# Kernel tuning notes

Measured on AMD Instinct MI355X. Metric: run time of the kernel, lower is better.

Reference implementation:

```python
import jax, jax.numpy as jnp
import numpy as np

N, E, B = 50000, 500000, 32
FEAT, HID, EDGE_DIM = 64, 128, 16
NUM_TASKS, TED, NCLS, TASKS_PER = 5000, 64, 3, 8
NLAYERS = 2


def setup_inputs() -> dict:
    key = jax.random.key(0)
    ks = jax.random.split(key, 20)
    s = 0.05
    inp = {
        "h": jax.random.normal(ks[0], (N, FEAT), jnp.float32),
        "x": jax.random.normal(ks[1], (N, 3), jnp.float32),
        "edge_index": jax.random.randint(ks[2], (2, E), 0, N, dtype=jnp.int32),
        "edge_attr": jax.random.normal(ks[3], (E, EDGE_DIM), jnp.float32),
        "batch": (jnp.arange(N, dtype=jnp.int32) * B // N).astype(jnp.int32),
        "tasks_indices": jnp.stack([
            jnp.repeat(jnp.arange(B, dtype=jnp.int32), TASKS_PER),
            jax.random.randint(ks[4], (B * TASKS_PER,), 0, NUM_TASKS, dtype=jnp.int32),
        ], axis=1),
        "batch_size": B,
        "embed_W": jax.random.normal(ks[5], (FEAT, HID), jnp.float32) * s,
        "embed_b": jnp.zeros((HID,), jnp.float32),
        "res_W": jax.random.normal(ks[6], (NLAYERS, HID, HID), jnp.float32) * s,
        "msg_W": jax.random.normal(ks[7], (NLAYERS, 2 * HID + 1, HID), jnp.float32) * s,
        "msg_b": jnp.zeros((NLAYERS, HID), jnp.float32),
        "upd_W": jax.random.normal(ks[8], (NLAYERS, 2 * HID, HID), jnp.float32) * s,
        "upd_b": jnp.zeros((NLAYERS, HID), jnp.float32),
        "mlp_W0": jax.random.normal(ks[9], (HID + TED, HID), jnp.float32) * s,
        "mlp_b0": jnp.zeros((HID,), jnp.float32),
        "mlp_W1": jax.random.normal(ks[10], (HID, HID), jnp.float32) * s,
        "mlp_b1": jnp.zeros((HID,), jnp.float32),
        "mlp_W2": jax.random.normal(ks[11], (HID, HID), jnp.float32) * s,
        "mlp_b2": jnp.zeros((HID,), jnp.float32),
        "mlp_W3": jax.random.normal(ks[12], (HID, NCLS), jnp.float32) * s,
        "mlp_b3": jnp.zeros((NCLS,), jnp.float32),
        "task_emb": jax.random.normal(ks[13], (NUM_TASKS, TED), jnp.float32),
    }
    return inp


def reference(h, x, edge_index, edge_attr, batch, tasks_indices, batch_size,
              embed_W, embed_b, res_W, msg_W, msg_b, upd_W, upd_b,
              mlp_W0, mlp_b0, mlp_W1, mlp_b1, mlp_W2, mlp_b2, mlp_W3, mlp_b3,
              task_emb):
    n = h.shape[0]
    row, col = edge_index[0], edge_index[1]
    # squared distances, identical across MP layers (positions never updated)
    dist = jnp.sum((x[row] - x[col]) ** 2, axis=1, keepdims=True)  # [E,1]
    emb = h @ embed_W + embed_b  # [N,HID]
    for l in range(NLAYERS):
        msg_in = jnp.concatenate([emb[row], emb[col], dist], axis=-1)  # [E,2H+1]
        msg = jax.nn.relu(msg_in @ msg_W[l] + msg_b[l])                # [E,H]
        aggr = jax.ops.segment_sum(msg, col, num_segments=n)           # [N,H]
        upd = jax.nn.relu(jnp.concatenate([emb, aggr], axis=-1) @ upd_W[l] + upd_b[l])
        emb = emb @ res_W[l] + upd
    # global mean pool per graph
    counts = jax.ops.segment_sum(jnp.ones((n,), emb.dtype), batch, num_segments=batch_size)
    pooled = jax.ops.segment_sum(emb, batch, num_segments=batch_size) / jnp.maximum(counts, 1.0)[:, None]
    # per-(protein, task) head; rows ordered as in the original dict-over-batch loop
    proto = tasks_indices[:, 0]
    tid = tasks_indices[:, 1]
    feat = jnp.concatenate([pooled[proto], task_emb[tid]], axis=-1)  # [K, H+TED]
    z = jax.nn.relu(feat @ mlp_W0 + mlp_b0)
    z = jax.nn.relu(z @ mlp_W1 + mlp_b1)
    z = jax.nn.relu(z @ mlp_W2 + mlp_b2)
    return z @ mlp_W3 + mlp_b3  # [K, NCLS]
```

## Files before the change

### kernel.cpp

```cpp
#include <hip/hip_runtime.h>

constexpr int NN = 50000;
constexpr int NE = 500000;
constexpr int NB = 32;
constexpr int NTROWS = 256;
constexpr int SCB = 196;
constexpr int NBLK64 = (NN + 63) / 64;

typedef __attribute__((ext_vector_type(8))) short bf16x8;
typedef __attribute__((ext_vector_type(4))) float f32x4;

static __device__ __forceinline__ unsigned short f2bf(float f) {
  unsigned u = __float_as_uint(f);
  unsigned r = (u + 0x7FFFu + ((u >> 16) & 1u)) >> 16;
  return (unsigned short)r;
}
static __device__ __forceinline__ float bf2f(unsigned short s) {
  return __uint_as_float(((unsigned)s) << 16);
}

__global__ void k_wprep(const float* __restrict__ msgW, const float* __restrict__ updW,
                        const float* __restrict__ resW, const float* __restrict__ embW,
                        unsigned short* __restrict__ wbf, int* __restrict__ cnt) {
  int idx = blockIdx.x * 256 + threadIdx.x;
  if (idx < NN) cnt[idx] = 0;
  if (idx >= 10 * 16384 + 8192) return;
  if (idx < 10 * 16384) {
    int m = idx >> 14, e = idx & 16383;
    int nn = e >> 7, kk = e & 127;
    int l = m / 5, t = m % 5;
    const float* src;
    if (t == 0)      src = msgW + (size_t)l * 257 * 128;
    else if (t == 1) src = msgW + (size_t)l * 257 * 128 + 128 * 128;
    else if (t == 2) src = updW + (size_t)l * 256 * 128;
    else if (t == 3) src = updW + (size_t)l * 256 * 128 + 128 * 128;
    else             src = resW + (size_t)l * 128 * 128;
    wbf[idx] = f2bf(src[kk * 128 + nn]);
  } else {
    int e = idx - 10 * 16384;
    int nn = e >> 6, kk = e & 63;
    wbf[idx] = f2bf(embW[kk * 128 + nn]);
  }
}

__global__ void k_count_gstart(const int* __restrict__ col, int* __restrict__ cnt,
                               const int* __restrict__ batch, int* __restrict__ gstart) {
  int e = blockIdx.x * 256 + threadIdx.x;
  if (e < NE) atomicAdd(&cnt[col[e]], 1);
  if (e < NN) {
    int b = batch[e];
    if (e == 0) gstart[b] = 0;
    else if (batch[e - 1] != b) gstart[b] = e;
    if (e == NN - 1) gstart[b + 1] = NN;
  }
}

__global__ __launch_bounds__(256) void k_scan1(const int* __restrict__ cnt,
                                               int* __restrict__ starts,
                                               int* __restrict__ bsum) {
  __shared__ int s[256];
  int t = threadIdx.x;
  int i = blockIdx.x * 256 + t;
  int v = (i < NN) ? cnt[i] : 0;
  s[t] = v; __syncthreads();
  for (int off = 1; off < 256; off <<= 1) {
    int u = (t >= off) ? s[t - off] : 0;
    __syncthreads();
    s[t] += u;
    __syncthreads();
  }
  if (i < NN) starts[i] = s[t] - v;
  if (t == 255) bsum[blockIdx.x] = s[255];
}

__global__ __launch_bounds__(256) void k_scan2(int* __restrict__ bsum) {
  __shared__ int s[256];
  int t = threadIdx.x;
  int v = (t < SCB) ? bsum[t] : 0;
  s[t] = v; __syncthreads();
  for (int off = 1; off < 256; off <<= 1) {
    int u = (t >= off) ? s[t - off] : 0;
    __syncthreads();
    s[t] += u;
    __syncthreads();
  }
  if (t < SCB) bsum[t] = s[t] - v;
}

__global__ __launch_bounds__(256) void k_scan3(int* __restrict__ starts,
                                               const int* __restrict__ bsum,
                                               int* __restrict__ cursor) {
  int i = blockIdx.x * 256 + threadIdx.x;
  if (i < NN) {
    int v = starts[i] + bsum[blockIdx.x];
    starts[i] = v;
    cursor[i] = v;
  }
  if (i == 0) starts[NN] = NE;
}

__global__ void k_scatter(const int* __restrict__ row, const int* __restrict__ col,
                          const float* __restrict__ x,
                          int* __restrict__ cursor, int2* __restrict__ spack) {
  int e = blockIdx.x * blockDim.x + threadIdx.x;
  if (e >= NE) return;
  int r = row[e], c = col[e];
  float dx = x[3*r+0] - x[3*c+0];
  float dy = x[3*r+1] - x[3*c+1];
  float dz = x[3*r+2] - x[3*c+2];
  float d = dx*dx + dy*dy + dz*dz;
  int pos = atomicAdd(&cursor[c], 1);
  spack[pos] = make_int2(r, __float_as_int(d));
}

static __device__ __forceinline__ void stage_tile64(
    unsigned short* lds, const unsigned short* __restrict__ src, int row0, int n, int tid) {
  #pragma unroll
  for (int ch = tid; ch < 1024; ch += 256) {
    int r = ch >> 4, kc = ch & 15;
    bf16x8 v = {0,0,0,0,0,0,0,0};
    if (row0 + r < n) v = *(const bf16x8*)(src + (size_t)(row0 + r) * 128 + kc * 8);
    int byte = (r * 256 + kc * 16) ^ ((r & 7) << 4);
    *(bf16x8*)((char*)lds + byte) = v;
  }
}

static __device__ __forceinline__ void vstore_tile64(
    unsigned short* __restrict__ dst, const unsigned short* lds, int row0, int n, int tid) {
  #pragma unroll
  for (int ch = tid; ch < 1024; ch += 256) {
    int r = ch >> 4, kc = ch & 15;
    if (row0 + r < n) {
      bf16x8 v = *(const bf16x8*)((const char*)lds + ((r * 256 + kc * 16) ^ ((r & 7) << 4)));
      *(bf16x8*)(dst + (size_t)(row0 + r) * 128 + kc * 8) = v;
    }
  }
}

static __device__ __forceinline__ void epi_to_lds64(
    unsigned short* lds, const f32x4 (&acc)[4][2], int lane, int c0) {
  int ccol = lane & 15, crow4 = (lane >> 4) * 4;
  #pragma unroll
  for (int ct = 0; ct < 2; ++ct) {
    int cc = c0 + ct * 16 + ccol;
    #pragma unroll
    for (int rt = 0; rt < 4; ++rt)
      #pragma unroll
      for (int j = 0; j < 4; ++j) {
        int lrow = rt * 16 + crow4 + j;
        int lbyte = (lrow * 256 + cc * 2) ^ ((lrow & 7) << 4);
        *(unsigned short*)((char*)lds + lbyte) = f2bf(acc[rt][ct][j]);
      }
  }
}

__global__ __launch_bounds__(256) void k_embed_dual(
    const float* __restrict__ h, const unsigned short* __restrict__ embWt,
    const float* __restrict__ embB,
    const unsigned short* __restrict__ W1t, const unsigned short* __restrict__ W2t,
    unsigned short* __restrict__ emb, unsigned short* __restrict__ Y1,
    unsigned short* __restrict__ Y2, int n) {
  __shared__ unsigned short Hs[64 * 64];
  __shared__ unsigned short Xs[64 * 128];
  __shared__ unsigned short Y1s[64 * 128];
  __shared__ unsigned short Y2s[64 * 128];
  int row0 = blockIdx.x * 64;
  int tid = threadIdx.x;
  int wave = tid >> 6, lane = tid & 63;
  int c0 = wave * 32;
  int arow = lane & 15, kb = (lane >> 4) * 8;
  {
    #pragma unroll
    for (int ch = tid; ch < 512; ch += 256) {
      int r = ch >> 3, kc = ch & 7;
      union { bf16x8 v; unsigned short s[8]; } u;
      if (row0 + r < n) {
        const float* p = h + (size_t)(row0 + r) * 64 + kc * 8;
        float4 f0 = *(const float4*)p, f1 = *(const float4*)(p + 4);
        u.s[0]=f2bf(f0.x); u.s[1]=f2bf(f0.y); u.s[2]=f2bf(f0.z); u.s[3]=f2bf(f0.w);
        u.s[4]=f2bf(f1.x); u.s[5]=f2bf(f1.y); u.s[6]=f2bf(f1.z); u.s[7]=f2bf(f1.w);
      } else {
        #pragma unroll
        for (int j = 0; j < 8; ++j) u.s[j] = 0;
      }
      int byte = (r * 128 + kc * 16) ^ ((r & 7) << 4);
      *(bf16x8*)((char*)Hs + byte) = u.v;
    }
  }
  float bB[2];
  #pragma unroll
  for (int ct = 0; ct < 2; ++ct) bB[ct] = embB[c0 + ct * 16 + (lane & 15)];
  __syncthreads();
  f32x4 accE[4][2] = {};
  #pragma unroll
  for (int ks = 0; ks < 2; ++ks) {
    bf16x8 a[4];
    #pragma unroll
    for (int rt = 0; rt < 4; ++rt) {
      int r = rt * 16 + arow;
      int byte = (r * 128 + (ks * 32 + kb) * 2) ^ ((r & 7) << 4);
      a[rt] = *(const bf16x8*)((const char*)Hs + byte);
    }
    #pragma unroll
    for (int ct = 0; ct < 2; ++ct) {
      bf16x8 b = *(const bf16x8*)(embWt + (size_t)(c0 + ct * 16 + arow) * 64 + ks * 32 + kb);
      #pragma unroll
      for (int rt = 0; rt < 4; ++rt)
        accE[rt][ct] = __builtin_amdgcn_mfma_f32_16x16x32_bf16(a[rt], b, accE[rt][ct], 0, 0, 0);
    }
  }
  {
    int ccol = lane & 15, crow4 = (lane >> 4) * 4;
    #pragma unroll
    for (int ct = 0; ct < 2; ++ct) {
      int cc = c0 + ct * 16 + ccol;
      #pragma unroll
      for (int rt = 0; rt < 4; ++rt)
        #pragma unroll
        for (int j = 0; j < 4; ++j) {
          int lrow = rt * 16 + crow4 + j;
          int lbyte = (lrow * 256 + cc * 2) ^ ((lrow & 7) << 4);
          *(unsigned short*)((char*)Xs + lbyte) = f2bf(accE[rt][ct][j] + bB[ct]);
        }
    }
  }
  __syncthreads();
  f32x4 acc1[4][2] = {};
  f32x4 acc2[4][2] = {};
  #pragma unroll
  for (int ks = 0; ks < 4; ++ks) {
    int k0 = ks * 32;
    bf16x8 a[4];
    #pragma unroll
    for (int rt = 0; rt < 4; ++rt) {
      int r = rt * 16 + arow;
      int byte = (r * 256 + (k0 + kb) * 2) ^ ((r & 7) << 4);
      a[rt] = *(const bf16x8*)((const char*)Xs + byte);
    }
    #pragma unroll
    for (int ct = 0; ct < 2; ++ct) {
      int col = c0 + ct * 16 + arow;
      bf16x8 b1 = *(const bf16x8*)(W1t + (size_t)col * 128 + k0 + kb);
      bf16x8 b2 = *(const bf16x8*)(W2t + (size_t)col * 128 + k0 + kb);
      #pragma unroll
      for (int rt = 0; rt < 4; ++rt) {
        acc1[rt][ct] = __builtin_amdgcn_mfma_f32_16x16x32_bf16(a[rt], b1, acc1[rt][ct], 0, 0, 0);
        acc2[rt][ct] = __builtin_amdgcn_mfma_f32_16x16x32_bf16(a[rt], b2, acc2[rt][ct], 0, 0, 0);
      }
    }
  }
  vstore_tile64(emb, Xs, row0, n, tid);
  epi_to_lds64(Y1s, acc1, lane, c0);
  epi_to_lds64(Y2s, acc2, lane, c0);
  __syncthreads();
  vstore_tile64(Y1, Y1s, row0, n, tid);
  vstore_tile64(Y2, Y2s, row0, n, tid);
}

__global__ __launch_bounds__(256) void k_node_dual(
    const unsigned short* __restrict__ emb, const unsigned short* __restrict__ aggr,
    const unsigned short* __restrict__ U1t, const unsigned short* __restrict__ U2t,
    const unsigned short* __restrict__ Rt, const float* __restrict__ updb,
    const unsigned short* __restrict__ W1t, const unsigned short* __restrict__ W2t,
    unsigned short* __restrict__ out, unsigned short* __restrict__ Y1,
    unsigned short* __restrict__ Y2, int n) {
  __shared__ unsigned short Es[64 * 128];
  __shared__ unsigned short As[64 * 128];
  __shared__ unsigned short Xs[64 * 128];
  int row0 = blockIdx.x * 64;
  int tid = threadIdx.x;
  int wave = tid >> 6, lane = tid & 63;
  int c0 = wave * 32;
  int arow = lane & 15, kb = (lane >> 4) * 8;
  stage_tile64(Es, emb,  row0, n, tid);
  stage_tile64(As, aggr, row0, n, tid);
  float uB[2];
  #pragma unroll
  for (int ct = 0; ct < 2; ++ct) uB[ct] = updb[c0 + ct * 16 + (lane & 15)];
  __syncthreads();
  f32x4 accU[4][2] = {};
  f32x4 accR[4][2] = {};
  #pragma unroll
  for (int ks = 0; ks < 4; ++ks) {
    int k0 = ks * 32;
    bf16x8 aE[4], aA[4];
    #pragma unroll
    for (int rt = 0; rt < 4; ++rt) {
      int r = rt * 16 + arow;
      int byte = (r * 256 + (k0 + kb) * 2) ^ ((r & 7) << 4);
      aE[rt] = *(const bf16x8*)((const char*)Es + byte);
      aA[rt] = *(const bf16x8*)((const char*)As + byte);
    }
    #pragma unroll
    for (int ct = 0; ct < 2; ++ct) {
      int col = c0 + ct * 16 + arow;
      bf16x8 bU1 = *(const bf16x8*)(U1t + (size_t)col * 128 + k0 + kb);
      bf16x8 bU2 = *(const bf16x8*)(U2t + (size_t)col * 128 + k0 + kb);
      bf16x8 bR  = *(const bf16x8*)(Rt  + (size_t)col * 128 + k0 + kb);
      #pragma unroll
      for (int rt = 0; rt < 4; ++rt) {
        accU[rt][ct] = __builtin_amdgcn_mfma_f32_16x16x32_bf16(aE[rt], bU1, accU[rt][ct], 0, 0, 0);
        accU[rt][ct] = __builtin_amdgcn_mfma_f32_16x16x32_bf16(aA[rt], bU2, accU[rt][ct], 0, 0, 0);
        accR[rt][ct] = __builtin_amdgcn_mfma_f32_16x16x32_bf16(aE[rt], bR,  accR[rt][ct], 0, 0, 0);
      }
    }
  }
  {
    int ccol = lane & 15, crow4 = (lane >> 4) * 4;
    #pragma unroll
    for (int ct = 0; ct < 2; ++ct) {
      int cc = c0 + ct * 16 + ccol;
      #pragma unroll
      for (int rt = 0; rt < 4; ++rt)
        #pragma unroll
        for (int j = 0; j < 4; ++j) {
          int lrow = rt * 16 + crow4 + j;
          int lbyte = (lrow * 256 + cc * 2) ^ ((lrow & 7) << 4);
          *(unsigned short*)((char*)Xs + lbyte) =
              f2bf(accR[rt][ct][j] + fmaxf(accU[rt][ct][j] + uB[ct], 0.f));
        }
    }
  }
  __syncthreads();
  f32x4 acc1[4][2] = {};
  f32x4 acc2[4][2] = {};
  #pragma unroll
  for (int ks = 0; ks < 4; ++ks) {
    int k0 = ks * 32;
    bf16x8 a[4];
    #pragma unroll
    for (int rt = 0; rt < 4; ++rt) {
      int r = rt * 16 + arow;
      int byte = (r * 256 + (k0 + kb) * 2) ^ ((r & 7) << 4);
      a[rt] = *(const bf16x8*)((const char*)Xs + byte);
    }
    #pragma unroll
    for (int ct = 0; ct < 2; ++ct) {
      int col = c0 + ct * 16 + arow;
      bf16x8 b1 = *(const bf16x8*)(W1t + (size_t)col * 128 + k0 + kb);
      bf16x8 b2 = *(const bf16x8*)(W2t + (size_t)col * 128 + k0 + kb);
      #pragma unroll
      for (int rt = 0; rt < 4; ++rt) {
        acc1[rt][ct] = __builtin_amdgcn_mfma_f32_16x16x32_bf16(a[rt], b1, acc1[rt][ct], 0, 0, 0);
        acc2[rt][ct] = __builtin_amdgcn_mfma_f32_16x16x32_bf16(a[rt], b2, acc2[rt][ct], 0, 0, 0);
      }
    }
  }
  vstore_tile64(out, Xs, row0, n, tid);
  epi_to_lds64(Es, acc1, lane, c0);
  epi_to_lds64(As, acc2, lane, c0);
  __syncthreads();
  vstore_tile64(Y1, Es, row0, n, tid);
  vstore_tile64(Y2, As, row0, n, tid);
}

__global__ __launch_bounds__(256) void k_node_pool(
    const unsigned short* __restrict__ emb, const unsigned short* __restrict__ aggr,
    const unsigned short* __restrict__ U1t, const unsigned short* __restrict__ U2t,
    const unsigned short* __restrict__ Rt, const float* __restrict__ updb,
    const int* __restrict__ batch,
    float* __restrict__ ppart, int* __restrict__ pgid, int n) {
  __shared__ unsigned short Es[64 * 128];
  __shared__ unsigned short As[64 * 128];
  __shared__ float Vs[64][128];
  __shared__ int sbat[64];
  int row0 = blockIdx.x * 64;
  int tid = threadIdx.x;
  int wave = tid >> 6, lane = tid & 63;
  int c0 = wave * 32;
  int arow = lane & 15, kb = (lane >> 4) * 8;
  stage_tile64(Es, emb,  row0, n, tid);
  stage_tile64(As, aggr, row0, n, tid);
  if (tid < 64) sbat[tid] = batch[min(row0 + tid, n - 1)];
  float uB[2];
  #pragma unroll
  for (int ct = 0; ct < 2; ++ct) uB[ct] = updb[c0 + ct * 16 + (lane & 15)];
  __syncthreads();
  f32x4 accU[4][2] = {};
  f32x4 accR[4][2] = {};
  #pragma unroll
  for (int ks = 0; ks < 4; ++ks) {
    int k0 = ks * 32;
    bf16x8 aE[4], aA[4];
    #pragma unroll
    for (int rt = 0; rt < 4; ++rt) {
      int r = rt * 16 + arow;
      int byte = (r * 256 + (k0 + kb) * 2) ^ ((r & 7) << 4);
      aE[rt] = *(const bf16x8*)((const char*)Es + byte);
      aA[rt] = *(const bf16x8*)((const char*)As + byte);
    }
    #pragma unroll
    for (int ct = 0; ct < 2; ++ct) {
      int col = c0 + ct * 16 + arow;
      bf16x8 bU1 = *(const bf16x8*)(U1t + (size_t)col * 128 + k0 + kb);
      bf16x8 bU2 = *(const bf16x8*)(U2t + (size_t)col * 128 + k0 + kb);
      bf16x8 bR  = *(const bf16x8*)(Rt  + (size_t)col * 128 + k0 + kb);
      #pragma unroll
      for (int rt = 0; rt < 4; ++rt) {
        accU[rt][ct] = __builtin_amdgcn_mfma_f32_16x16x32_bf16(aE[rt], bU1, accU[rt][ct], 0, 0, 0);
        accU[rt][ct] = __builtin_amdgcn_mfma_f32_16x16x32_bf16(aA[rt], bU2, accU[rt][ct], 0, 0, 0);
        accR[rt][ct] = __builtin_amdgcn_mfma_f32_16x16x32_bf16(aE[rt], bR,  accR[rt][ct], 0, 0, 0);
      }
    }
  }
  int ccol = lane & 15, crow4 = (lane >> 4) * 4;
  #pragma unroll
  for (int ct = 0; ct < 2; ++ct) {
    int cc = c0 + ct * 16 + ccol;
    #pragma unroll
    for (int rt = 0; rt < 4; ++rt)
      #pragma unroll
      for (int j = 0; j < 4; ++j) {
        int lrow = rt * 16 + crow4 + j;
        Vs[lrow][cc] = accR[rt][ct][j] + fmaxf(accU[rt][ct][j] + uB[ct], 0.f);
      }
  }
  __syncthreads();
  if (tid < 128) {
    int g0 = sbat[0];
    float a0 = 0.f, a1 = 0.f;
    #pragma unroll 4
    for (int r = 0; r < 64; ++r) {
      if (row0 + r < n) {
        float v = Vs[r][tid];
        if (sbat[r] == g0) a0 += v; else a1 += v;
      }
    }
    ppart[(size_t)(2 * blockIdx.x) * 128 + tid] = a0;
    ppart[(size_t)(2 * blockIdx.x + 1) * 128 + tid] = a1;
    if (tid == 0) {
      int gl = sbat[63];
      pgid[2 * blockIdx.x] = g0;
      pgid[2 * blockIdx.x + 1] = (gl != g0) ? gl : -1;
    }
  }
}

__global__ __launch_bounds__(256) void k_aggr_pull(
    const int* __restrict__ starts, const int2* __restrict__ spack,
    const unsigned short* __restrict__ A, const unsigned short* __restrict__ Bm,
    const float* __restrict__ wd, const float* __restrict__ mb,
    unsigned short* __restrict__ aggr) {
  int t = blockIdx.x * 256 + threadIdx.x;
  int node = t >> 4;
  if (node >= NN) return;
  int c0 = (t & 15) * 8;
  union { bf16x8 v; unsigned short s[8]; } ub;
  ub.v = *(const bf16x8*)(Bm + (size_t)node * 128 + c0);
  float4 w0 = *(const float4*)(wd + c0), w1 = *(const float4*)(wd + c0 + 4);
  float4 bb0 = *(const float4*)(mb + c0), bb1 = *(const float4*)(mb + c0 + 4);
  float wv[8]   = {w0.x, w0.y, w0.z, w0.w, w1.x, w1.y, w1.z, w1.w};
  float bv[8]   = {bb0.x, bb0.y, bb0.z, bb0.w, bb1.x, bb1.y, bb1.z, bb1.w};
  float basev[8], accv[8];
  #pragma unroll
  for (int j = 0; j < 8; ++j) { basev[j] = bf2f(ub.s[j]) + bv[j]; accv[j] = 0.f; }
  int s = starts[node], e = starts[node + 1];
  int i = s;
  for (; i + 4 <= e; i += 4) {
    int2 p0 = spack[i + 0], p1 = spack[i + 1];
    int2 p2 = spack[i + 2], p3 = spack[i + 3];
    union { bf16x8 v; unsigned short s[8]; } a0, a1, a2, a3;
    a0.v = *(const bf16x8*)(A + (size_t)p0.x * 128 + c0);
    a1.v = *(const bf16x8*)(A + (size_t)p1.x * 128 + c0);
    a2.v = *(const bf16x8*)(A + (size_t)p2.x * 128 + c0);
    a3.v = *(const bf16x8*)(A + (size_t)p3.x * 128 + c0);
    float d0 = __int_as_float(p0.y), d1 = __int_as_float(p1.y);
    float d2 = __int_as_float(p2.y), d3 = __int_as_float(p3.y);
    #pragma unroll
    for (int j = 0; j < 8; ++j) {
      accv[j] += fmaxf(bf2f(a0.s[j]) + fmaf(d0, wv[j], basev[j]), 0.f);
      accv[j] += fmaxf(bf2f(a1.s[j]) + fmaf(d1, wv[j], basev[j]), 0.f);
      accv[j] += fmaxf(bf2f(a2.s[j]) + fmaf(d2, wv[j], basev[j]), 0.f);
      accv[j] += fmaxf(bf2f(a3.s[j]) + fmaf(d3, wv[j], basev[j]), 0.f);
    }
  }
  for (; i < e; ++i) {
    int2 p = spack[i];
    union { bf16x8 v; unsigned short s[8]; } a;
    a.v = *(const bf16x8*)(A + (size_t)p.x * 128 + c0);
    float d = __int_as_float(p.y);
    #pragma unroll
    for (int j = 0; j < 8; ++j)
      accv[j] += fmaxf(bf2f(a.s[j]) + fmaf(d, wv[j], basev[j]), 0.f);
  }
  union { bf16x8 v; unsigned short s[8]; } o;
  #pragma unroll
  for (int j = 0; j < 8; ++j) o.s[j] = f2bf(accv[j]);
  *(bf16x8*)(aggr + (size_t)node * 128 + c0) = o.v;
}

__global__ __launch_bounds__(128) void k_pool2(const float* __restrict__ ppart,
                                               const int* __restrict__ pgid,
                                               const int* __restrict__ gstart,
                                               float* __restrict__ pooled) {
  int g = blockIdx.x, t = threadIdx.x;
  int blo = gstart[g] >> 6;
  int bhi = (gstart[g + 1] - 1) >> 6;
  float acc = 0.f;
  for (int b = blo; b <= bhi; ++b) {
    if (pgid[2 * b] == g)     acc += ppart[(size_t)(2 * b) * 128 + t];
    if (pgid[2 * b + 1] == g) acc += ppart[(size_t)(2 * b + 1) * 128 + t];
  }
  float cntf = (float)(gstart[g + 1] - gstart[g]);
  pooled[g * 128 + t] = acc / fmaxf(cntf, 1.f);
}

__global__ __launch_bounds__(128) void k_head(
    const float* __restrict__ pooled, const float* __restrict__ temb,
    const int* __restrict__ tasks,
    const float* __restrict__ W0, const float* __restrict__ b0,
    const float* __restrict__ W1, const float* __restrict__ b1,
    const float* __restrict__ W2, const float* __restrict__ b2,
    const float* __restrict__ W3, const float* __restrict__ b3,
    float* __restrict__ out) {
  __shared__ float f[192];
  __shared__ float za[128];
  __shared__ float zb[128];
  int rowi = blockIdx.x, t = threadIdx.x;
  int proto = tasks[rowi*2 + 0];
  int tid2  = tasks[rowi*2 + 1];
  f[t] = pooled[proto*128 + t];
  if (t < 64) f[128 + t] = temb[(size_t)tid2*64 + t];
  __syncthreads();
  float a = b0[t];
  for (int k = 0; k < 192; ++k) a += f[k] * W0[k*128 + t];
  za[t] = fmaxf(a, 0.f);
  __syncthreads();
  a = b1[t];
  for (int k = 0; k < 128; ++k) a += za[k] * W1[k*128 + t];
  zb[t] = fmaxf(a, 0.f);
  __syncthreads();
  a = b2[t];
  for (int k = 0; k < 128; ++k) a += zb[k] * W2[k*128 + t];
  za[t] = fmaxf(a, 0.f);
  __syncthreads();
  if (t < 3) {
    a = b3[t];
    for (int k = 0; k < 128; ++k) a += za[k] * W3[k*3 + t];
    out[rowi*3 + t] = a;
  }
}

extern "C" void kernel_launch(void* const* d_in, const int* in_sizes, int n_in,
                              void* d_out, int out_size, void* d_ws, size_t ws_size,
                              hipStream_t stream) {
  const float* h    = (const float*)d_in[0];
  const float* x    = (const float*)d_in[1];
  const int*   ei   = (const int*)d_in[2];
  const int*   batch= (const int*)d_in[4];
  const int*   tasks= (const int*)d_in[5];
  const float* embW = (const float*)d_in[7];
  const float* embB = (const float*)d_in[8];
  const float* resW = (const float*)d_in[9];
  const float* msgW = (const float*)d_in[10];
  const float* msgB = (const float*)d_in[11];
  const float* updW = (const float*)d_in[12];
  const float* updB = (const float*)d_in[13];
  const float* W0 = (const float*)d_in[14]; const float* b0 = (const float*)d_in[15];
  const float* W1 = (const float*)d_in[16]; const float* b1 = (const float*)d_in[17];
  const float* W2 = (const float*)d_in[18]; const float* b2 = (const float*)d_in[19];
  const float* W3 = (const float*)d_in[20]; const float* b3 = (const float*)d_in[21];
  const float* temb = (const float*)d_in[22];
  const int* row = ei;
  const int* col = ei + NE;

  unsigned short* bws = (unsigned short*)d_ws;
  unsigned short* e0   = bws;  bws += (size_t)NN*128;
  unsigned short* e1   = bws;  bws += (size_t)NN*128;
  unsigned short* Abuf = bws;  bws += (size_t)NN*128;
  unsigned short* Bbuf = bws;  bws += (size_t)NN*128;
  unsigned short* wbf  = bws;  bws += 10*16384 + 8192;
  float* ws = (float*)bws;
  float* pooled= ws;  ws += NB*128;
  float* ppart = ws;  ws += (size_t)2*NBLK64*128;
  int2*  spack = (int2*)ws;
  int*   iws   = (int*)(spack + NE);
  int*   cnt    = iws;  iws += NN;
  int*   starts = iws;  iws += NN + 1;
  int*   cursor = iws;  iws += NN;
  int*   gstart = iws;  iws += NB + 1;
  int*   bsum   = iws;  iws += 256;
  int*   pgid   = iws;  iws += 2*NBLK64;

  const unsigned short* embWt = wbf + (size_t)10*16384;

  k_wprep<<<672, 256, 0, stream>>>(msgW, updW, resW, embW, wbf, cnt);

  k_count_gstart<<<(NE + 255)/256, 256, 0, stream>>>(col, cnt, batch, gstart);
  k_scan1<<<SCB, 256, 0, stream>>>(cnt, starts, bsum);
  k_scan2<<<1, 256, 0, stream>>>(bsum);
  k_scan3<<<SCB, 256, 0, stream>>>(starts, bsum, cursor);
  k_scatter<<<(NE + 255)/256, 256, 0, stream>>>(row, col, x, cursor, spack);

  const unsigned short* m0W1t = wbf + (size_t)0 * 16384;
  const unsigned short* m0W2t = wbf + (size_t)1 * 16384;
  const unsigned short* u0W1t = wbf + (size_t)2 * 16384;
  const unsigned short* u0W2t = wbf + (size_t)3 * 16384;
  const unsigned short* r0Wt  = wbf + (size_t)4 * 16384;
  const unsigned short* m1W1t = wbf + (size_t)5 * 16384;
  const unsigned short* m1W2t = wbf + (size_t)6 * 16384;
  const unsigned short* u1W1t = wbf + (size_t)7 * 16384;
  const unsigned short* u1W2t = wbf + (size_t)8 * 16384;
  const unsigned short* r1Wt  = wbf + (size_t)9 * 16384;

  k_embed_dual<<<NBLK64, 256, 0, stream>>>(h, embWt, embB, m0W1t, m0W2t,
                                           e0, Abuf, Bbuf, NN);
  k_aggr_pull<<<(NN*16 + 255)/256, 256, 0, stream>>>(starts, spack, Abuf, Bbuf,
                                                     msgW + 256*128, msgB, e1);
  k_node_dual<<<NBLK64, 256, 0, stream>>>(e0, e1, u0W1t, u0W2t, r0Wt, updB,
                                          m1W1t, m1W2t, e1, Abuf, Bbuf, NN);
  k_aggr_pull<<<(NN*16 + 255)/256, 256, 0, stream>>>(starts, spack, Abuf, Bbuf,
                                                     msgW + (size_t)257*128 + 256*128,
                                                     msgB + 128, e0);
  k_node_pool<<<NBLK64, 256, 0, stream>>>(e1, e0, u1W1t, u1W2t, r1Wt, updB + 128,
                                          batch, ppart, pgid, NN);
  k_pool2<<<NB, 128, 0, stream>>>(ppart, pgid, gstart, pooled);
  k_head<<<NTROWS, 128, 0, stream>>>(pooled, temb, tasks,
                                     W0, b0, W1, b1, W2, b2, W3, b3, (float*)d_out);
}
```

Baseline: 226.5 us.

## Use 8 waves per 64-row node tile and pool via wave shuffles

```diff
diff --git a/kernel.cpp b/kernel.cpp
--- a/kernel.cpp
+++ b/kernel.cpp
@@ -113,10 +113,11 @@
   spack[pos] = make_int2(r, __float_as_int(d));
 }
 
+template<int TPB>
 static __device__ __forceinline__ void stage_tile64(
     unsigned short* lds, const unsigned short* __restrict__ src, int row0, int n, int tid) {
   #pragma unroll
-  for (int ch = tid; ch < 1024; ch += 256) {
+  for (int ch = tid; ch < 1024; ch += TPB) {
     int r = ch >> 4, kc = ch & 15;
     bf16x8 v = {0,0,0,0,0,0,0,0};
     if (row0 + r < n) v = *(const bf16x8*)(src + (size_t)(row0 + r) * 128 + kc * 8);
@@ -125,10 +126,11 @@
   }
 }
 
+template<int TPB>
 static __device__ __forceinline__ void vstore_tile64(
     unsigned short* __restrict__ dst, const unsigned short* lds, int row0, int n, int tid) {
   #pragma unroll
-  for (int ch = tid; ch < 1024; ch += 256) {
+  for (int ch = tid; ch < 1024; ch += TPB) {
     int r = ch >> 4, kc = ch & 15;
     if (row0 + r < n) {
       bf16x8 v = *(const bf16x8*)((const char*)lds + ((r * 256 + kc * 16) ^ ((r & 7) << 4)));
@@ -138,23 +140,20 @@
 }
 
 static __device__ __forceinline__ void epi_to_lds64(
-    unsigned short* lds, const f32x4 (&acc)[4][2], int lane, int c0) {
+    unsigned short* lds, const f32x4 (&acc)[4], int lane, int c0) {
   int ccol = lane & 15, crow4 = (lane >> 4) * 4;
-  #pragma unroll
-  for (int ct = 0; ct < 2; ++ct) {
-    int cc = c0 + ct * 16 + ccol;
-    #pragma unroll
-    for (int rt = 0; rt < 4; ++rt)
-      #pragma unroll
-      for (int j = 0; j < 4; ++j) {
-        int lrow = rt * 16 + crow4 + j;
-        int lbyte = (lrow * 256 + cc * 2) ^ ((lrow & 7) << 4);
-        *(unsigned short*)((char*)lds + lbyte) = f2bf(acc[rt][ct][j]);
-      }
-  }
-}
-
-__global__ __launch_bounds__(256) void k_embed_dual(
+  int cc = c0 + ccol;
+  #pragma unroll
+  for (int rt = 0; rt < 4; ++rt)
+    #pragma unroll
+    for (int j = 0; j < 4; ++j) {
+      int lrow = rt * 16 + crow4 + j;
+      int lbyte = (lrow * 256 + cc * 2) ^ ((lrow & 7) << 4);
+      *(unsigned short*)((char*)lds + lbyte) = f2bf(acc[rt][j]);
+    }
+}
+
+__global__ __launch_bounds__(512) void k_embed_dual(
     const float* __restrict__ h, const unsigned short* __restrict__ embWt,
     const float* __restrict__ embB,
     const unsigned short* __restrict__ W1t, const unsigned short* __restrict__ W2t,
@@ -167,97 +166,75 @@
   int row0 = blockIdx.x * 64;
   int tid = threadIdx.x;
   int wave = tid >> 6, lane = tid & 63;
-  int c0 = wave * 32;
+  int c0 = wave * 16;
   int arow = lane & 15, kb = (lane >> 4) * 8;
   {
-    #pragma unroll
-    for (int ch = tid; ch < 512; ch += 256) {
-      int r = ch >> 3, kc = ch & 7;
-      union { bf16x8 v; unsigned short s[8]; } u;
-      if (row0 + r < n) {
-        const float* p = h + (size_t)(row0 + r) * 64 + kc * 8;
-        float4 f0 = *(const float4*)p, f1 = *(const float4*)(p + 4);
-        u.s[0]=f2bf(f0.x); u.s[1]=f2bf(f0.y); u.s[2]=f2bf(f0.z); u.s[3]=f2bf(f0.w);
-        u.s[4]=f2bf(f1.x); u.s[5]=f2bf(f1.y); u.s[6]=f2bf(f1.z); u.s[7]=f2bf(f1.w);
-      } else {
-        #pragma unroll
-        for (int j = 0; j < 8; ++j) u.s[j] = 0;
-      }
-      int byte = (r * 128 + kc * 16) ^ ((r & 7) << 4);
-      *(bf16x8*)((char*)Hs + byte) = u.v;
-    }
-  }
-  float bB[2];
-  #pragma unroll
-  for (int ct = 0; ct < 2; ++ct) bB[ct] = embB[c0 + ct * 16 + (lane & 15)];
-  __syncthreads();
-  f32x4 accE[4][2] = {};
+    int r = tid >> 3, kc = tid & 7;
+    union { bf16x8 v; unsigned short s[8]; } u;
+    if (row0 + r < n) {
+      const float* p = h + (size_t)(row0 + r) * 64 + kc * 8;
+      float4 f0 = *(const float4*)p, f1 = *(const float4*)(p + 4);
+      u.s[0]=f2bf(f0.x); u.s[1]=f2bf(f0.y); u.s[2]=f2bf(f0.z); u.s[3]=f2bf(f0.w);
+      u.s[4]=f2bf(f1.x); u.s[5]=f2bf(f1.y); u.s[6]=f2bf(f1.z); u.s[7]=f2bf(f1.w);
+    } else {
+      #pragma unroll
+      for (int j = 0; j < 8; ++j) u.s[j] = 0;
+    }
+    int byte = (r * 128 + kc * 16) ^ ((r & 7) << 4);
+    *(bf16x8*)((char*)Hs + byte) = u.v;
+  }
+  float bB = embB[c0 + (lane & 15)];
+  __syncthreads();
+  f32x4 accE[4] = {};
   #pragma unroll
   for (int ks = 0; ks < 2; ++ks) {
-    bf16x8 a[4];
+    bf16x8 b = *(const bf16x8*)(embWt + (size_t)(c0 + arow) * 64 + ks * 32 + kb);
     #pragma unroll
     for (int rt = 0; rt < 4; ++rt) {
       int r = rt * 16 + arow;
       int byte = (r * 128 + (ks * 32 + kb) * 2) ^ ((r & 7) << 4);
-      a[rt] = *(const bf16x8*)((const char*)Hs + byte);
-    }
-    #pragma unroll
-    for (int ct = 0; ct < 2; ++ct) {
-      bf16x8 b = *(const bf16x8*)(embWt + (size_t)(c0 + ct * 16 + arow) * 64 + ks * 32 + kb);
-      #pragma unroll
-      for (int rt = 0; rt < 4; ++rt)
-        accE[rt][ct] = __builtin_amdgcn_mfma_f32_16x16x32_bf16(a[rt], b, accE[rt][ct], 0, 0, 0);
+      bf16x8 a = *(const bf16x8*)((const char*)Hs + byte);
+      accE[rt] = __builtin_amdgcn_mfma_f32_16x16x32_bf16(a, b, accE[rt], 0, 0, 0);
     }
   }
   {
     int ccol = lane & 15, crow4 = (lane >> 4) * 4;
-    #pragma unroll
-    for (int ct = 0; ct < 2; ++ct) {
-      int cc = c0 + ct * 16 + ccol;
+    int cc = c0 + ccol;
+    #pragma unroll
+    for (int rt = 0; rt < 4; ++rt)
       #pragma unroll
-      for (int rt = 0; rt < 4; ++rt)
-        #pragma unroll
-        for (int j = 0; j < 4; ++j) {
-          int lrow = rt * 16 + crow4 + j;
-          int lbyte = (lrow * 256 + cc * 2) ^ ((lrow & 7) << 4);
-          *(unsigned short*)((char*)Xs + lbyte) = f2bf(accE[rt][ct][j] + bB[ct]);
-        }
-    }
-  }
-  __syncthreads();
-  f32x4 acc1[4][2] = {};
-  f32x4 acc2[4][2] = {};
+      for (int j = 0; j < 4; ++j) {
+        int lrow = rt * 16 + crow4 + j;
+        int lbyte = (lrow * 256 + cc * 2) ^ ((lrow & 7) << 4);
+        *(unsigned short*)((char*)Xs + lbyte) = f2bf(accE[rt][j] + bB);
+      }
+  }
+  __syncthreads();
+  f32x4 acc1[4] = {};
+  f32x4 acc2[4] = {};
   #pragma unroll
   for (int ks = 0; ks < 4; ++ks) {
     int k0 = ks * 32;
-    bf16x8 a[4];
+    bf16x8 b1 = *(const bf16x8*)(W1t + (size_t)(c0 + arow) * 128 + k0 + kb);
+    bf16x8 b2 = *(const bf16x8*)(W2t + (size_t)(c0 + arow) * 128 + k0 + kb);
     #pragma unroll
     for (int rt = 0; rt < 4; ++rt) {
       int r = rt * 16 + arow;
       int byte = (r * 256 + (k0 + kb) * 2) ^ ((r & 7) << 4);
-      a[rt] = *(const bf16x8*)((const char*)Xs + byte);
-    }
-    #pragma unroll
-    for (int ct = 0; ct < 2; ++ct) {
-      int col = c0 + ct * 16 + arow;
-      bf16x8 b1 = *(const bf16x8*)(W1t + (size_t)col * 128 + k0 + kb);
-      bf16x8 b2 = *(const bf16x8*)(W2t + (size_t)col * 128 + k0 + kb);
-      #pragma unroll
-      for (int rt = 0; rt < 4; ++rt) {
-        acc1[rt][ct] = __builtin_amdgcn_mfma_f32_16x16x32_bf16(a[rt], b1, acc1[rt][ct], 0, 0, 0);
-        acc2[rt][ct] = __builtin_amdgcn_mfma_f32_16x16x32_bf16(a[rt], b2, acc2[rt][ct], 0, 0, 0);
-      }
-    }
-  }
-  vstore_tile64(emb, Xs, row0, n, tid);
+      bf16x8 a = *(const bf16x8*)((const char*)Xs + byte);
+      acc1[rt] = __builtin_amdgcn_mfma_f32_16x16x32_bf16(a, b1, acc1[rt], 0, 0, 0);
+      acc2[rt] = __builtin_amdgcn_mfma_f32_16x16x32_bf16(a, b2, acc2[rt], 0, 0, 0);
+    }
+  }
+  vstore_tile64<512>(emb, Xs, row0, n, tid);
   epi_to_lds64(Y1s, acc1, lane, c0);
   epi_to_lds64(Y2s, acc2, lane, c0);
   __syncthreads();
-  vstore_tile64(Y1, Y1s, row0, n, tid);
-  vstore_tile64(Y2, Y2s, row0, n, tid);
-}
-
-__global__ __launch_bounds__(256) void k_node_dual(
+  vstore_tile64<512>(Y1, Y1s, row0, n, tid);
+  vstore_tile64<512>(Y2, Y2s, row0, n, tid);
+}
+
+__global__ __launch_bounds__(512) void k_node_dual(
     const unsigned short* __restrict__ emb, const unsigned short* __restrict__ aggr,
     const unsigned short* __restrict__ U1t, const unsigned short* __restrict__ U2t,
     const unsigned short* __restrict__ Rt, const float* __restrict__ updb,
@@ -270,91 +247,70 @@
   int row0 = blockIdx.x * 64;
   int tid = threadIdx.x;
   int wave = tid >> 6, lane = tid & 63;
-  int c0 = wave * 32;
+  int c0 = wave * 16;
   int arow = lane & 15, kb = (lane >> 4) * 8;
-  stage_tile64(Es, emb,  row0, n, tid);
-  stage_tile64(As, aggr, row0, n, tid);
-  float uB[2];
-  #pragma unroll
-  for (int ct = 0; ct < 2; ++ct) uB[ct] = updb[c0 + ct * 16 + (lane & 15)];
-  __syncthreads();
-  f32x4 accU[4][2] = {};
-  f32x4 accR[4][2] = {};
+  stage_tile64<512>(Es, emb,  row0, n, tid);
+  stage_tile64<512>(As, aggr, row0, n, tid);
+  float uB = updb[c0 + (lane & 15)];
+  __syncthreads();
+  f32x4 accU[4] = {};
+  f32x4 accR[4] = {};
   #pragma unroll
   for (int ks = 0; ks < 4; ++ks) {
     int k0 = ks * 32;
-    bf16x8 aE[4], aA[4];
+    bf16x8 bU1 = *(const bf16x8*)(U1t + (size_t)(c0 + arow) * 128 + k0 + kb);
+    bf16x8 bU2 = *(const bf16x8*)(U2t + (size_t)(c0 + arow) * 128 + k0 + kb);
+    bf16x8 bR  = *(const bf16x8*)(Rt  + (size_t)(c0 + arow) * 128 + k0 + kb);
     #pragma unroll
     for (int rt = 0; rt < 4; ++rt) {
       int r = rt * 16 + arow;
       int byte = (r * 256 + (k0 + kb) * 2) ^ ((r & 7) << 4);
-      aE[rt] = *(const bf16x8*)((const char*)Es + byte);
-      aA[rt] = *(const bf16x8*)((const char*)As + byte);
-    }
-    #pragma unroll
-    for (int ct = 0; ct < 2; ++ct) {
-      int col = c0 + ct * 16 + arow;
-      bf16x8 bU1 = *(const bf16x8*)(U1t + (size_t)col * 128 + k0 + kb);
-      bf16x8 bU2 = *(const bf16x8*)(U2t + (size_t)col * 128 + k0 + kb);
-      bf16x8 bR  = *(const bf16x8*)(Rt  + (size_t)col * 128 + k0 + kb);
-      #pragma unroll
-      for (int rt = 0; rt < 4; ++rt) {
-        accU[rt][ct] = __builtin_amdgcn_mfma_f32_16x16x32_bf16(aE[rt], bU1, accU[rt][ct], 0, 0, 0);
-        accU[rt][ct] = __builtin_amdgcn_mfma_f32_16x16x32_bf16(aA[rt], bU2, accU[rt][ct], 0, 0, 0);
-        accR[rt][ct] = __builtin_amdgcn_mfma_f32_16x16x32_bf16(aE[rt], bR,  accR[rt][ct], 0, 0, 0);
-      }
+      bf16x8 aE = *(const bf16x8*)((const char*)Es + byte);
+      bf16x8 aA = *(const bf16x8*)((const char*)As + byte);
+      accU[rt] = __builtin_amdgcn_mfma_f32_16x16x32_bf16(aE, bU1, accU[rt], 0, 0, 0);
+      accU[rt] = __builtin_amdgcn_mfma_f32_16x16x32_bf16(aA, bU2, accU[rt], 0, 0, 0);
+      accR[rt] = __builtin_amdgcn_mfma_f32_16x16x32_bf16(aE, bR,  accR[rt], 0, 0, 0);
     }
   }
   {
     int ccol = lane & 15, crow4 = (lane >> 4) * 4;
-    #pragma unroll
-    for (int ct = 0; ct < 2; ++ct) {
-      int cc = c0 + ct * 16 + ccol;
+    int cc = c0 + ccol;
+    #pragma unroll
+    for (int rt = 0; rt < 4; ++rt)
       #pragma unroll
-      for (int rt = 0; rt < 4; ++rt)
-        #pragma unroll
-        for (int j = 0; j < 4; ++j) {
-          int lrow = rt * 16 + crow4 + j;
-          int lbyte = (lrow * 256 + cc * 2) ^ ((lrow & 7) << 4);
-          *(unsigned short*)((char*)Xs + lbyte) =
-              f2bf(accR[rt][ct][j] + fmaxf(accU[rt][ct][j] + uB[ct], 0.f));
-        }
-    }
-  }
-  __syncthreads();
-  f32x4 acc1[4][2] = {};
-  f32x4 acc2[4][2] = {};
+      for (int j = 0; j < 4; ++j) {
+        int lrow = rt * 16 + crow4 + j;
+        int lbyte = (lrow * 256 + cc * 2) ^ ((lrow & 7) << 4);
+        *(unsigned short*)((char*)Xs + lbyte) =
+            f2bf(accR[rt][j] + fmaxf(accU[rt][j] + uB, 0.f));
+      }
+  }
+  __syncthreads();
+  f32x4 acc1[4] = {};
+  f32x4 acc2[4] = {};
   #pragma unroll
   for (int ks = 0; ks < 4; ++ks) {
     int k0 = ks * 32;
-    bf16x8 a[4];
+    bf16x8 b1 = *(const bf16x8*)(W1t + (size_t)(c0 + arow) * 128 + k0 + kb);
+    bf16x8 b2 = *(const bf16x8*)(W2t + (size_t)(c0 + arow) * 128 + k0 + kb);
     #pragma unroll
     for (int rt = 0; rt < 4; ++rt) {
       int r = rt * 16 + arow;
       int byte = (r * 256 + (k0 + kb) * 2) ^ ((r & 7) << 4);
-      a[rt] = *(const bf16x8*)((const char*)Xs + byte);
-    }
-    #pragma unroll
-    for (int ct = 0; ct < 2; ++ct) {
-      int col = c0 + ct * 16 + arow;
-      bf16x8 b1 = *(const bf16x8*)(W1t + (size_t)col * 128 + k0 + kb);
-      bf16x8 b2 = *(const bf16x8*)(W2t + (size_t)col * 128 + k0 + kb);
-      #pragma unroll
-      for (int rt = 0; rt < 4; ++rt) {
-        acc1[rt][ct] = __builtin_amdgcn_mfma_f32_16x16x32_bf16(a[rt], b1, acc1[rt][ct], 0, 0, 0);
-        acc2[rt][ct] = __builtin_amdgcn_mfma_f32_16x16x32_bf16(a[rt], b2, acc2[rt][ct], 0, 0, 0);
-      }
-    }
-  }
-  vstore_tile64(out, Xs, row0, n, tid);
+      bf16x8 a = *(const bf16x8*)((const char*)Xs + byte);
+      acc1[rt] = __builtin_amdgcn_mfma_f32_16x16x32_bf16(a, b1, acc1[rt], 0, 0, 0);
+      acc2[rt] = __builtin_amdgcn_mfma_f32_16x16x32_bf16(a, b2, acc2[rt], 0, 0, 0);
+    }
+  }
+  vstore_tile64<512>(out, Xs, row0, n, tid);
   epi_to_lds64(Es, acc1, lane, c0);
   epi_to_lds64(As, acc2, lane, c0);
   __syncthreads();
-  vstore_tile64(Y1, Es, row0, n, tid);
-  vstore_tile64(Y2, As, row0, n, tid);
-}
-
-__global__ __launch_bounds__(256) void k_node_pool(
+  vstore_tile64<512>(Y1, Es, row0, n, tid);
+  vstore_tile64<512>(Y2, As, row0, n, tid);
+}
+
+__global__ __launch_bounds__(512) void k_node_pool(
     const unsigned short* __restrict__ emb, const unsigned short* __restrict__ aggr,
     const unsigned short* __restrict__ U1t, const unsigned short* __restrict__ U2t,
     const unsigned short* __restrict__ Rt, const float* __restrict__ updb,
@@ -362,77 +318,60 @@
     float* __restrict__ ppart, int* __restrict__ pgid, int n) {
   __shared__ unsigned short Es[64 * 128];
   __shared__ unsigned short As[64 * 128];
-  __shared__ float Vs[64][128];
   __shared__ int sbat[64];
   int row0 = blockIdx.x * 64;
   int tid = threadIdx.x;
   int wave = tid >> 6, lane = tid & 63;
-  int c0 = wave * 32;
+  int c0 = wave * 16;
   int arow = lane & 15, kb = (lane >> 4) * 8;
-  stage_tile64(Es, emb,  row0, n, tid);
-  stage_tile64(As, aggr, row0, n, tid);
+  stage_tile64<512>(Es, emb,  row0, n, tid);
+  stage_tile64<512>(As, aggr, row0, n, tid);
   if (tid < 64) sbat[tid] = batch[min(row0 + tid, n - 1)];
-  float uB[2];
-  #pragma unroll
-  for (int ct = 0; ct < 2; ++ct) uB[ct] = updb[c0 + ct * 16 + (lane & 15)];
-  __syncthreads();
-  f32x4 accU[4][2] = {};
-  f32x4 accR[4][2] = {};
+  float uB = updb[c0 + (lane & 15)];
+  __syncthreads();
+  f32x4 accU[4] = {};
+  f32x4 accR[4] = {};
   #pragma unroll
   for (int ks = 0; ks < 4; ++ks) {
     int k0 = ks * 32;
-    bf16x8 aE[4], aA[4];
+    bf16x8 bU1 = *(const bf16x8*)(U1t + (size_t)(c0 + arow) * 128 + k0 + kb);
+    bf16x8 bU2 = *(const bf16x8*)(U2t + (size_t)(c0 + arow) * 128 + k0 + kb);
+    bf16x8 bR  = *(const bf16x8*)(Rt  + (size_t)(c0 + arow) * 128 + k0 + kb);
     #pragma unroll
     for (int rt = 0; rt < 4; ++rt) {
       int r = rt * 16 + arow;
       int byte = (r * 256 + (k0 + kb) * 2) ^ ((r & 7) << 4);
-      aE[rt] = *(const bf16x8*)((const char*)Es + byte);
-      aA[rt] = *(const bf16x8*)((const char*)As + byte);
-    }
-    #pragma unroll
-    for (int ct = 0; ct < 2; ++ct) {
-      int col = c0 + ct * 16 + arow;
-      bf16x8 bU1 = *(const bf16x8*)(U1t + (size_t)col * 128 + k0 + kb);
-      bf16x8 bU2 = *(const bf16x8*)(U2t + (size_t)col * 128 + k0 + kb);
-      bf16x8 bR  = *(const bf16x8*)(Rt  + (size_t)col * 128 + k0 + kb);
-      #pragma unroll
-      for (int rt = 0; rt < 4; ++rt) {
-        accU[rt][ct] = __builtin_amdgcn_mfma_f32_16x16x32_bf16(aE[rt], bU1, accU[rt][ct], 0, 0, 0);
-        accU[rt][ct] = __builtin_amdgcn_mfma_f32_16x16x32_bf16(aA[rt], bU2, accU[rt][ct], 0, 0, 0);
-        accR[rt][ct] = __builtin_amdgcn_mfma_f32_16x16x32_bf16(aE[rt], bR,  accR[rt][ct], 0, 0, 0);
+      bf16x8 aE = *(const bf16x8*)((const char*)Es + byte);
+      bf16x8 aA = *(const bf16x8*)((const char*)As + byte);
+      accU[rt] = __builtin_amdgcn_mfma_f32_16x16x32_bf16(aE, bU1, accU[rt], 0, 0, 0);
+      accU[rt] = __builtin_amdgcn_mfma_f32_16x16x32_bf16(aA, bU2, accU[rt], 0, 0, 0);
+      accR[rt] = __builtin_amdgcn_mfma_f32_16x16x32_bf16(aE, bR,  accR[rt], 0, 0, 0);
+    }
+  }
+  int g0 = sbat[0];
+  int crow4 = (lane >> 4) * 4;
+  float s0 = 0.f, s1 = 0.f;
+  #pragma unroll
+  for (int rt = 0; rt < 4; ++rt)
+    #pragma unroll
+    for (int j = 0; j < 4; ++j) {
+      int lrow = rt * 16 + crow4 + j;
+      if (row0 + lrow < n) {
+        float v = accR[rt][j] + fmaxf(accU[rt][j] + uB, 0.f);
+        if (sbat[lrow] == g0) s0 += v; else s1 += v;
       }
     }
-  }
-  int ccol = lane & 15, crow4 = (lane >> 4) * 4;
-  #pragma unroll
-  for (int ct = 0; ct < 2; ++ct) {
-    int cc = c0 + ct * 16 + ccol;
-    #pragma unroll
-    for (int rt = 0; rt < 4; ++rt)
-      #pragma unroll
-      for (int j = 0; j < 4; ++j) {
-        int lrow = rt * 16 + crow4 + j;
-        Vs[lrow][cc] = accR[rt][ct][j] + fmaxf(accU[rt][ct][j] + uB[ct], 0.f);
-      }
-  }
-  __syncthreads();
-  if (tid < 128) {
-    int g0 = sbat[0];
-    float a0 = 0.f, a1 = 0.f;
-    #pragma unroll 4
-    for (int r = 0; r < 64; ++r) {
-      if (row0 + r < n) {
-        float v = Vs[r][tid];
-        if (sbat[r] == g0) a0 += v; else a1 += v;
-      }
-    }
-    ppart[(size_t)(2 * blockIdx.x) * 128 + tid] = a0;
-    ppart[(size_t)(2 * blockIdx.x + 1) * 128 + tid] = a1;
-    if (tid == 0) {
-      int gl = sbat[63];
-      pgid[2 * blockIdx.x] = g0;
-      pgid[2 * blockIdx.x + 1] = (gl != g0) ? gl : -1;
-    }
+  s0 += __shfl_xor(s0, 16); s0 += __shfl_xor(s0, 32);
+  s1 += __shfl_xor(s1, 16); s1 += __shfl_xor(s1, 32);
+  if ((lane >> 4) == 0) {
+    int cc = c0 + (lane & 15);
+    ppart[(size_t)(2 * blockIdx.x) * 128 + cc] = s0;
+    ppart[(size_t)(2 * blockIdx.x + 1) * 128 + cc] = s1;
+  }
+  if (tid == 0) {
+    int gl = sbat[63];
+    pgid[2 * blockIdx.x] = g0;
+    pgid[2 * blockIdx.x + 1] = (gl != g0) ? gl : -1;
   }
 }
 
@@ -603,16 +542,16 @@
   const unsigned short* u1W2t = wbf + (size_t)8 * 16384;
   const unsigned short* r1Wt  = wbf + (size_t)9 * 16384;
 
-  k_embed_dual<<<NBLK64, 256, 0, stream>>>(h, embWt, embB, m0W1t, m0W2t,
+  k_embed_dual<<<NBLK64, 512, 0, stream>>>(h, embWt, embB, m0W1t, m0W2t,
                                            e0, Abuf, Bbuf, NN);
   k_aggr_pull<<<(NN*16 + 255)/256, 256, 0, stream>>>(starts, spack, Abuf, Bbuf,
                                                      msgW + 256*128, msgB, e1);
-  k_node_dual<<<NBLK64, 256, 0, stream>>>(e0, e1, u0W1t, u0W2t, r0Wt, updB,
+  k_node_dual<<<NBLK64, 512, 0, stream>>>(e0, e1, u0W1t, u0W2t, r0Wt, updB,
                                           m1W1t, m1W2t, e1, Abuf, Bbuf, NN);
   k_aggr_pull<<<(NN*16 + 255)/256, 256, 0, stream>>>(starts, spack, Abuf, Bbuf,
                                                      msgW + (size_t)257*128 + 256*128,
                                                      msgB + 128, e0);
-  k_node_pool<<<NBLK64, 256, 0, stream>>>(e1, e0, u1W1t, u1W2t, r1Wt, updB + 128,
+  k_node_pool<<<NBLK64, 512, 0, stream>>>(e1, e0, u1W1t, u1W2t, r1Wt, updB + 128,
                                           batch, ppart, pgid, NN);
   k_pool2<<<NB, 128, 0, stream>>>(ppart, pgid, gstart, pooled);
   k_head<<<NTROWS, 128, 0, stream>>>(pooled, temb, tasks,
```

Result: faster. 213.6 us (-5.7%).
